# Performance work log

Hardware: AMD Instinct MI355X
Metric: run time of the kernel (lower is better)

Reference implementation:

```python
import jax, jax.numpy as jnp
import numpy as np

B, Q, KV = 4, 256, 1024
QS, KS, H, VS = 128, 128, 128, 256

def setup_inputs() -> dict:
    key = jax.random.key(0)
    ks = jax.random.split(key, 7)
    return {
        "queries": jax.random.normal(ks[0], (B, Q, QS), dtype=jnp.float32),
        "keys": jax.random.normal(ks[1], (B, KV, KS), dtype=jnp.float32),
        "values": jax.random.normal(ks[2], (B, KV, VS), dtype=jnp.float32),
        "valid_lens": jax.random.randint(ks[3], (B,), 0, KV, dtype=jnp.int64 if jax.config.read('jax_enable_x64') else jnp.int32),
        "Wq": jax.random.normal(ks[4], (QS, H), dtype=jnp.float32),
        "Wk": jax.random.normal(ks[5], (KS, H), dtype=jnp.float32),
        "wv": jax.random.normal(ks[6], (H,), dtype=jnp.float32),
    }

def reference(queries, keys, values, valid_lens, Wq, Wk, wv):
    # project: [B,Q,H], [B,KV,H]
    q = jnp.einsum('bqd,dh->bqh', queries, Wq)
    k = jnp.einsum('bkd,dh->bkh', keys, Wk)
    # additive scores: broadcast add -> tanh -> reduce with w_v  [B,Q,KV]
    feats = jnp.tanh(q[:, :, None, :] + k[:, None, :, :])  # [B,Q,KV,H]
    scores = jnp.einsum('bqkh,h->bqk', feats, wv)
    # masked softmax over KV with value -1e6 at masked slots
    mask = jnp.arange(scores.shape[-1])[None, None, :] < valid_lens[:, None, None]
    scores = jnp.where(mask, scores, -1e6)
    attn = jax.nn.softmax(scores, axis=-1)
    # weighted sum of values  [B,Q,VS]
    return jnp.einsum('bqk,bkv->bqv', attn, values)
```

## Files before the change

### kernel.cpp

```cpp
#include <hip/hip_runtime.h>

#define C2LOG2E 2.8853900817779268f
#define LOG2E   1.4426950408889634f

__device__ __forceinline__ float sig2(float x) {
    return __builtin_amdgcn_rcpf(__builtin_amdgcn_exp2f(x) + 1.0f);
}

__global__ __launch_bounds__(256) void proj_kernel(
    const float* __restrict__ q_in, const float* __restrict__ k_in,
    const float* __restrict__ Wq, const float* __restrict__ Wk,
    float* __restrict__ qc, float* __restrict__ kct)
{
    __shared__ __align__(16) float x_s[8][128];
    __shared__ float ps[2][8][128];
    int tid = threadIdx.x;
    int blk = blockIdx.x;
    bool is_q = (blk < 128);
    int r0 = (is_q ? blk : blk - 128) * 8;
    const float* X = (is_q ? q_in : k_in) + (size_t)r0 * 128;
    const float* W = is_q ? Wq : Wk;

    {
        float4 v = ((const float4*)X)[tid];
        *(float4*)&x_s[tid >> 5][(tid & 31) * 4] = v;
    }
    __syncthreads();

    int h    = tid & 127;
    int half = tid >> 7;
    int d0   = half * 64;
    float acc[8] = {0,0,0,0,0,0,0,0};
#pragma unroll 2
    for (int i4 = 0; i4 < 16; ++i4) {
        int d = d0 + 4*i4;
        float w0 = W[(d+0)*128 + h];
        float w1 = W[(d+1)*128 + h];
        float w2 = W[(d+2)*128 + h];
        float w3 = W[(d+3)*128 + h];
#pragma unroll
        for (int r = 0; r < 8; ++r) {
            float4 xv = *(const float4*)&x_s[r][d];
            acc[r] = fmaf(xv.x, w0, fmaf(xv.y, w1,
                     fmaf(xv.z, w2, fmaf(xv.w, w3, acc[r]))));
        }
    }
#pragma unroll
    for (int r = 0; r < 8; ++r) ps[half][r][h] = acc[r];
    __syncthreads();

    int rq = tid >> 7;
    float v0 = (ps[0][rq*4+0][h] + ps[1][rq*4+0][h]) * C2LOG2E;
    float v1 = (ps[0][rq*4+1][h] + ps[1][rq*4+1][h]) * C2LOG2E;
    float v2 = (ps[0][rq*4+2][h] + ps[1][rq*4+2][h]) * C2LOG2E;
    float v3 = (ps[0][rq*4+3][h] + ps[1][rq*4+3][h]) * C2LOG2E;

    if (is_q) {
        qc[(size_t)(r0 + rq*4 + 0)*128 + h] = v0;
        qc[(size_t)(r0 + rq*4 + 1)*128 + h] = v1;
        qc[(size_t)(r0 + rq*4 + 2)*128 + h] = v2;
        qc[(size_t)(r0 + rq*4 + 3)*128 + h] = v3;
    } else {
        int bb = r0 >> 10;
        int c  = (r0 & 1023) >> 6;
        int i0 = (r0 & 63) + rq*4;
        float* dst = kct + ((((size_t)(bb*16 + c))*32 + (h >> 2))*64 + i0)*4 + (h & 3);
        dst[0]  = v0;
        dst[4]  = v1;
        dst[8]  = v2;
        dst[12] = v3;
    }
}

__global__ __launch_bounds__(1024, 4) void attn_kernel(
    const float* __restrict__ qc, const float* __restrict__ kct,
    const float* __restrict__ values, const int* __restrict__ valid_lens,
    const float* __restrict__ wv, float* __restrict__ out)
{
    __shared__ float2 e2_s[2][1024];
    __shared__ float4 po8[8][4][64];
    __shared__ float2 red_m[16], red_s[16];

    int tid  = threadIdx.x;
    int b    = blockIdx.y;
    int q0   = blockIdx.x * 4;
    int w    = tid >> 6;
    int lane = tid & 63;
    int qh   = w >> 3;
    int c0   = w & 7;
    int vl   = valid_lens[b];

    const float4* qa4 = (const float4*)(qc + (size_t)(b*256 + q0 + 2*qh)*128);
    const float4* qb4 = qa4 + 32;
    const float4* wv4 = (const float4*)wv;
    const float4* kb  = (const float4*)kct;
    const float4* p0  = kb + ((size_t)(b*16 + c0))*2048 + lane;
    const float4* p1  = p0 + 8*2048;

    bool act0 = (c0*64 < vl);
    bool act1 = ((c0 + 8)*64 < vl);
    float a00=0.f, a10=0.f, a01=0.f, a11=0.f;

    if (act1) {
        for (int hb = 0; hb < 32; ++hb) {
            float4 wvv = wv4[hb];
            float4 qa = qa4[hb], qb = qb4[hb];
            float4 k0 = p0[(size_t)hb*64];
            float4 k1 = p1[(size_t)hb*64];
            a00 = fmaf(wvv.x, sig2(qa.x + k0.x), a00);
            a10 = fmaf(wvv.x, sig2(qb.x + k0.x), a10);
            a01 = fmaf(wvv.x, sig2(qa.x + k1.x), a01);
            a11 = fmaf(wvv.x, sig2(qb.x + k1.x), a11);
            a00 = fmaf(wvv.y, sig2(qa.y + k0.y), a00);
            a10 = fmaf(wvv.y, sig2(qb.y + k0.y), a10);
            a01 = fmaf(wvv.y, sig2(qa.y + k1.y), a01);
            a11 = fmaf(wvv.y, sig2(qb.y + k1.y), a11);
            a00 = fmaf(wvv.z, sig2(qa.z + k0.z), a00);
            a10 = fmaf(wvv.z, sig2(qb.z + k0.z), a10);
            a01 = fmaf(wvv.z, sig2(qa.z + k1.z), a01);
            a11 = fmaf(wvv.z, sig2(qb.z + k1.z), a11);
            a00 = fmaf(wvv.w, sig2(qa.w + k0.w), a00);
            a10 = fmaf(wvv.w, sig2(qb.w + k0.w), a10);
            a01 = fmaf(wvv.w, sig2(qa.w + k1.w), a01);
            a11 = fmaf(wvv.w, sig2(qb.w + k1.w), a11);
        }
    } else if (act0) {
        for (int hb = 0; hb < 32; ++hb) {
            float4 wvv = wv4[hb];
            float4 qa = qa4[hb], qb = qb4[hb];
            float4 k0 = p0[(size_t)hb*64];
            a00 = fmaf(wvv.x, sig2(qa.x + k0.x), a00);
            a10 = fmaf(wvv.x, sig2(qb.x + k0.x), a10);
            a00 = fmaf(wvv.y, sig2(qa.y + k0.y), a00);
            a10 = fmaf(wvv.y, sig2(qb.y + k0.y), a10);
            a00 = fmaf(wvv.z, sig2(qa.z + k0.z), a00);
            a10 = fmaf(wvv.z, sig2(qb.z + k0.z), a10);
            a00 = fmaf(wvv.w, sig2(qa.w + k0.w), a00);
            a10 = fmaf(wvv.w, sig2(qb.w + k0.w), a10);
        }
    }

    int kv0 = c0*64 + lane, kv1 = kv0 + 512;
    bool m0v = (kv0 < vl), m1v = (kv1 < vl);
    float s00 = m0v ? -2.f*a00 : -1e6f;
    float s10 = m0v ? -2.f*a10 : -1e6f;
    float s01 = m1v ? -2.f*a01 : -1e6f;
    float s11 = m1v ? -2.f*a11 : -1e6f;

    float m0 = fmaxf(s00, s01), m1 = fmaxf(s10, s11);
#pragma unroll
    for (int off = 32; off; off >>= 1) {
        m0 = fmaxf(m0, __shfl_xor(m0, off));
        m1 = fmaxf(m1, __shfl_xor(m1, off));
    }
    if (lane == 0) red_m[w] = make_float2(m0, m1);
    __syncthreads();
    {
        float2 mm = red_m[qh*8];
#pragma unroll
        for (int ww = 1; ww < 8; ++ww) {
            float2 t = red_m[qh*8 + ww];
            mm.x = fmaxf(mm.x, t.x); mm.y = fmaxf(mm.y, t.y);
        }
        m0 = mm.x; m1 = mm.y;
    }

    float e00 = __builtin_amdgcn_exp2f((s00 - m0) * LOG2E);
    float e10 = __builtin_amdgcn_exp2f((s10 - m1) * LOG2E);
    float e01 = __builtin_amdgcn_exp2f((s01 - m0) * LOG2E);
    float e11 = __builtin_amdgcn_exp2f((s11 - m1) * LOG2E);
    e2_s[qh][kv0] = make_float2(e00, e10);
    e2_s[qh][kv1] = make_float2(e01, e11);
    float l0 = e00 + e01, l1 = e10 + e11;
#pragma unroll
    for (int off = 32; off; off >>= 1) {
        l0 += __shfl_xor(l0, off);
        l1 += __shfl_xor(l1, off);
    }
    if (lane == 0) red_s[w] = make_float2(l0, l1);
    __syncthreads();

    int kv_end = (vl == 0) ? 1024 : vl;
    float4 ac[4] = {{0,0,0,0},{0,0,0,0},{0,0,0,0},{0,0,0,0}};
    const float4* V4 = (const float4*)values + (size_t)b*65536 + lane;
#pragma unroll 2
    for (int k2 = w; k2 < kv_end; k2 += 16) {
        float4 vv = V4[(size_t)k2*64];
        float2 ea = e2_s[0][k2];
        float2 eb = e2_s[1][k2];
        ac[0].x = fmaf(ea.x, vv.x, ac[0].x); ac[0].y = fmaf(ea.x, vv.y, ac[0].y);
        ac[0].z = fmaf(ea.x, vv.z, ac[0].z); ac[0].w = fmaf(ea.x, vv.w, ac[0].w);
        ac[1].x = fmaf(ea.y, vv.x, ac[1].x); ac[1].y = fmaf(ea.y, vv.y, ac[1].y);
        ac[1].z = fmaf(ea.y, vv.z, ac[1].z); ac[1].w = fmaf(ea.y, vv.w, ac[1].w);
        ac[2].x = fmaf(eb.x, vv.x, ac[2].x); ac[2].y = fmaf(eb.x, vv.y, ac[2].y);
        ac[2].z = fmaf(eb.x, vv.z, ac[2].z); ac[2].w = fmaf(eb.x, vv.w, ac[2].w);
        ac[3].x = fmaf(eb.y, vv.x, ac[3].x); ac[3].y = fmaf(eb.y, vv.y, ac[3].y);
        ac[3].z = fmaf(eb.y, vv.z, ac[3].z); ac[3].w = fmaf(eb.y, vv.w, ac[3].w);
    }

    if (w >= 8) {
#pragma unroll
        for (int q = 0; q < 4; ++q) po8[w-8][q][lane] = ac[q];
    }
    __syncthreads();
    if (w < 8) {
#pragma unroll
        for (int q = 0; q < 4; ++q) {
            float4 t = po8[w][q][lane];
            t.x += ac[q].x; t.y += ac[q].y; t.z += ac[q].z; t.w += ac[q].w;
            po8[w][q][lane] = t;
        }
    }
    __syncthreads();

    int qq  = tid >> 8;
    int col = tid & 255;
    float ssum = 0.f;
#pragma unroll
    for (int ww = 0; ww < 8; ++ww) {
        float2 t = red_s[(qq >> 1)*8 + ww];
        ssum += (qq & 1) ? t.y : t.x;
    }
    const float* pp = (const float*)po8;
    float r = 0.f;
#pragma unroll
    for (int ww = 0; ww < 8; ++ww) r += pp[(ww*4 + qq)*256 + col];
    out[((size_t)(b*256 + q0 + qq))*256 + col] = r / ssum;
}

extern "C" void kernel_launch(void* const* d_in, const int* in_sizes, int n_in,
                              void* d_out, int out_size, void* d_ws, size_t ws_size,
                              hipStream_t stream)
{
    const float* queries = (const float*)d_in[0];
    const float* keys    = (const float*)d_in[1];
    const float* values  = (const float*)d_in[2];
    const int*   vlens   = (const int*)d_in[3];
    const float* Wq      = (const float*)d_in[4];
    const float* Wk      = (const float*)d_in[5];
    const float* wv      = (const float*)d_in[6];
    float* out = (float*)d_out;

    float* qc  = (float*)d_ws;
    float* kct = qc + 4*256*128;

    proj_kernel<<<640, 256, 0, stream>>>(queries, keys, Wq, Wk, qc, kct);
    attn_kernel<<<dim3(64, 4), 1024, 0, stream>>>(qc, kct, values, vlens, wv, out);
}
```

Before: 103.2 us.

## Skip masked key projections, vectorize proj stores, halve attention block size

The projection kernel now returns early for key row-blocks beyond valid_len, skipping work whose scores are masked anyway. It also uses a 4-way split over input dimension with two output columns per thread, so results can be written as float4 stores in both the q and the transposed k layouts. The attention kernel goes from 1024-thread blocks covering 4 queries to 512-thread blocks covering 2 queries on a doubled grid, which drops the two-stage partial-sum reduction. The cost is that each V row is reread by twice as many blocks, and parallelism is restructured across the grid.

```diff
diff --git a/kernel.cpp b/kernel.cpp
--- a/kernel.cpp
+++ b/kernel.cpp
@@ -10,95 +10,95 @@
 __global__ __launch_bounds__(256) void proj_kernel(
     const float* __restrict__ q_in, const float* __restrict__ k_in,
     const float* __restrict__ Wq, const float* __restrict__ Wk,
+    const int* __restrict__ valid_lens,
     float* __restrict__ qc, float* __restrict__ kct)
 {
     __shared__ __align__(16) float x_s[8][128];
-    __shared__ float ps[2][8][128];
+    __shared__ __align__(16) float ps[4][8][128];
     int tid = threadIdx.x;
     int blk = blockIdx.x;
     bool is_q = (blk < 128);
     int r0 = (is_q ? blk : blk - 128) * 8;
+    int bb = r0 >> 10;
+    if (!is_q) {
+        int vl = valid_lens[bb];
+        if ((r0 & 1023) >= vl) return;
+    }
     const float* X = (is_q ? q_in : k_in) + (size_t)r0 * 128;
     const float* W = is_q ? Wq : Wk;
 
-    {
-        float4 v = ((const float4*)X)[tid];
-        *(float4*)&x_s[tid >> 5][(tid & 31) * 4] = v;
-    }
-    __syncthreads();
-
-    int h    = tid & 127;
-    int half = tid >> 7;
-    int d0   = half * 64;
-    float acc[8] = {0,0,0,0,0,0,0,0};
-#pragma unroll 2
-    for (int i4 = 0; i4 < 16; ++i4) {
-        int d = d0 + 4*i4;
-        float w0 = W[(d+0)*128 + h];
-        float w1 = W[(d+1)*128 + h];
-        float w2 = W[(d+2)*128 + h];
-        float w3 = W[(d+3)*128 + h];
+    *(float4*)&x_s[tid >> 5][(tid & 31) * 4] = ((const float4*)X)[tid];
+    __syncthreads();
+
+    int hl = tid & 63;
+    int dq = tid >> 6;
+    float a0[8] = {0,0,0,0,0,0,0,0};
+    float a1[8] = {0,0,0,0,0,0,0,0};
+#pragma unroll
+    for (int i4 = 0; i4 < 8; ++i4) {
+        int d = dq*32 + i4*4;
+        float w00 = W[(d+0)*128 + hl], w01 = W[(d+0)*128 + hl + 64];
+        float w10 = W[(d+1)*128 + hl], w11 = W[(d+1)*128 + hl + 64];
+        float w20 = W[(d+2)*128 + hl], w21 = W[(d+2)*128 + hl + 64];
+        float w30 = W[(d+3)*128 + hl], w31 = W[(d+3)*128 + hl + 64];
 #pragma unroll
         for (int r = 0; r < 8; ++r) {
             float4 xv = *(const float4*)&x_s[r][d];
-            acc[r] = fmaf(xv.x, w0, fmaf(xv.y, w1,
-                     fmaf(xv.z, w2, fmaf(xv.w, w3, acc[r]))));
-        }
-    }
-#pragma unroll
-    for (int r = 0; r < 8; ++r) ps[half][r][h] = acc[r];
-    __syncthreads();
-
-    int rq = tid >> 7;
-    float v0 = (ps[0][rq*4+0][h] + ps[1][rq*4+0][h]) * C2LOG2E;
-    float v1 = (ps[0][rq*4+1][h] + ps[1][rq*4+1][h]) * C2LOG2E;
-    float v2 = (ps[0][rq*4+2][h] + ps[1][rq*4+2][h]) * C2LOG2E;
-    float v3 = (ps[0][rq*4+3][h] + ps[1][rq*4+3][h]) * C2LOG2E;
-
+            a0[r] = fmaf(xv.x,w00, fmaf(xv.y,w10, fmaf(xv.z,w20, fmaf(xv.w,w30, a0[r]))));
+            a1[r] = fmaf(xv.x,w01, fmaf(xv.y,w11, fmaf(xv.z,w21, fmaf(xv.w,w31, a1[r]))));
+        }
+    }
+#pragma unroll
+    for (int r = 0; r < 8; ++r) {
+        ps[dq][r][hl]      = a0[r];
+        ps[dq][r][hl + 64] = a1[r];
+    }
+    __syncthreads();
+
+    int r  = tid >> 5;
+    int c4 = (tid & 31) * 4;
+    float4 s0 = *(const float4*)&ps[0][r][c4];
+    float4 s1 = *(const float4*)&ps[1][r][c4];
+    float4 s2 = *(const float4*)&ps[2][r][c4];
+    float4 s3 = *(const float4*)&ps[3][r][c4];
+    float4 v = make_float4(((s0.x+s1.x)+(s2.x+s3.x))*C2LOG2E,
+                           ((s0.y+s1.y)+(s2.y+s3.y))*C2LOG2E,
+                           ((s0.z+s1.z)+(s2.z+s3.z))*C2LOG2E,
+                           ((s0.w+s1.w)+(s2.w+s3.w))*C2LOG2E);
     if (is_q) {
-        qc[(size_t)(r0 + rq*4 + 0)*128 + h] = v0;
-        qc[(size_t)(r0 + rq*4 + 1)*128 + h] = v1;
-        qc[(size_t)(r0 + rq*4 + 2)*128 + h] = v2;
-        qc[(size_t)(r0 + rq*4 + 3)*128 + h] = v3;
+        *(float4*)&qc[(size_t)(r0 + r)*128 + c4] = v;
     } else {
-        int bb = r0 >> 10;
-        int c  = (r0 & 1023) >> 6;
-        int i0 = (r0 & 63) + rq*4;
-        float* dst = kct + ((((size_t)(bb*16 + c))*32 + (h >> 2))*64 + i0)*4 + (h & 3);
-        dst[0]  = v0;
-        dst[4]  = v1;
-        dst[8]  = v2;
-        dst[12] = v3;
-    }
-}
-
-__global__ __launch_bounds__(1024, 4) void attn_kernel(
+        int c    = (r0 & 1023) >> 6;
+        int kvin = (r0 & 63) + r;
+        *(float4*)&kct[((((size_t)(bb*16 + c))*32 + (c4 >> 2))*64 + kvin)*4] = v;
+    }
+}
+
+__global__ __launch_bounds__(512, 4) void attn_kernel(
     const float* __restrict__ qc, const float* __restrict__ kct,
     const float* __restrict__ values, const int* __restrict__ valid_lens,
     const float* __restrict__ wv, float* __restrict__ out)
 {
-    __shared__ float2 e2_s[2][1024];
-    __shared__ float4 po8[8][4][64];
-    __shared__ float2 red_m[16], red_s[16];
+    __shared__ float2 e2_s[1024];
+    __shared__ float4 po[8][2][64];
+    __shared__ float2 red_m[8], red_s[8];
 
     int tid  = threadIdx.x;
     int b    = blockIdx.y;
-    int q0   = blockIdx.x * 4;
+    int q0   = blockIdx.x * 2;
     int w    = tid >> 6;
     int lane = tid & 63;
-    int qh   = w >> 3;
-    int c0   = w & 7;
     int vl   = valid_lens[b];
 
-    const float4* qa4 = (const float4*)(qc + (size_t)(b*256 + q0 + 2*qh)*128);
+    const float4* qa4 = (const float4*)(qc + (size_t)(b*256 + q0)*128);
     const float4* qb4 = qa4 + 32;
     const float4* wv4 = (const float4*)wv;
     const float4* kb  = (const float4*)kct;
-    const float4* p0  = kb + ((size_t)(b*16 + c0))*2048 + lane;
+    const float4* p0  = kb + ((size_t)(b*16 + w))*2048 + lane;
     const float4* p1  = p0 + 8*2048;
 
-    bool act0 = (c0*64 < vl);
-    bool act1 = ((c0 + 8)*64 < vl);
+    bool act0 = (w*64 < vl);
+    bool act1 = ((w + 8)*64 < vl);
     float a00=0.f, a10=0.f, a01=0.f, a11=0.f;
 
     if (act1) {
@@ -140,7 +140,7 @@
         }
     }
 
-    int kv0 = c0*64 + lane, kv1 = kv0 + 512;
+    int kv0 = w*64 + lane, kv1 = kv0 + 512;
     bool m0v = (kv0 < vl), m1v = (kv1 < vl);
     float s00 = m0v ? -2.f*a00 : -1e6f;
     float s10 = m0v ? -2.f*a10 : -1e6f;
@@ -156,10 +156,10 @@
     if (lane == 0) red_m[w] = make_float2(m0, m1);
     __syncthreads();
     {
-        float2 mm = red_m[qh*8];
+        float2 mm = red_m[0];
 #pragma unroll
         for (int ww = 1; ww < 8; ++ww) {
-            float2 t = red_m[qh*8 + ww];
+            float2 t = red_m[ww];
             mm.x = fmaxf(mm.x, t.x); mm.y = fmaxf(mm.y, t.y);
         }
         m0 = mm.x; m1 = mm.y;
@@ -169,8 +169,8 @@
     float e10 = __builtin_amdgcn_exp2f((s10 - m1) * LOG2E);
     float e01 = __builtin_amdgcn_exp2f((s01 - m0) * LOG2E);
     float e11 = __builtin_amdgcn_exp2f((s11 - m1) * LOG2E);
-    e2_s[qh][kv0] = make_float2(e00, e10);
-    e2_s[qh][kv1] = make_float2(e01, e11);
+    e2_s[kv0] = make_float2(e00, e10);
+    e2_s[kv1] = make_float2(e01, e11);
     float l0 = e00 + e01, l1 = e10 + e11;
 #pragma unroll
     for (int off = 32; off; off >>= 1) {
@@ -181,36 +181,19 @@
     __syncthreads();
 
     int kv_end = (vl == 0) ? 1024 : vl;
-    float4 ac[4] = {{0,0,0,0},{0,0,0,0},{0,0,0,0},{0,0,0,0}};
+    float4 ac0 = {0,0,0,0}, ac1 = {0,0,0,0};
     const float4* V4 = (const float4*)values + (size_t)b*65536 + lane;
 #pragma unroll 2
-    for (int k2 = w; k2 < kv_end; k2 += 16) {
+    for (int k2 = w; k2 < kv_end; k2 += 8) {
         float4 vv = V4[(size_t)k2*64];
-        float2 ea = e2_s[0][k2];
-        float2 eb = e2_s[1][k2];
-        ac[0].x = fmaf(ea.x, vv.x, ac[0].x); ac[0].y = fmaf(ea.x, vv.y, ac[0].y);
-        ac[0].z = fmaf(ea.x, vv.z, ac[0].z); ac[0].w = fmaf(ea.x, vv.w, ac[0].w);
-        ac[1].x = fmaf(ea.y, vv.x, ac[1].x); ac[1].y = fmaf(ea.y, vv.y, ac[1].y);
-        ac[1].z = fmaf(ea.y, vv.z, ac[1].z); ac[1].w = fmaf(ea.y, vv.w, ac[1].w);
-        ac[2].x = fmaf(eb.x, vv.x, ac[2].x); ac[2].y = fmaf(eb.x, vv.y, ac[2].y);
-        ac[2].z = fmaf(eb.x, vv.z, ac[2].z); ac[2].w = fmaf(eb.x, vv.w, ac[2].w);
-        ac[3].x = fmaf(eb.y, vv.x, ac[3].x); ac[3].y = fmaf(eb.y, vv.y, ac[3].y);
-        ac[3].z = fmaf(eb.y, vv.z, ac[3].z); ac[3].w = fmaf(eb.y, vv.w, ac[3].w);
-    }
-
-    if (w >= 8) {
-#pragma unroll
-        for (int q = 0; q < 4; ++q) po8[w-8][q][lane] = ac[q];
-    }
-    __syncthreads();
-    if (w < 8) {
-#pragma unroll
-        for (int q = 0; q < 4; ++q) {
-            float4 t = po8[w][q][lane];
-            t.x += ac[q].x; t.y += ac[q].y; t.z += ac[q].z; t.w += ac[q].w;
-            po8[w][q][lane] = t;
-        }
-    }
+        float2 ee = e2_s[k2];
+        ac0.x = fmaf(ee.x, vv.x, ac0.x); ac0.y = fmaf(ee.x, vv.y, ac0.y);
+        ac0.z = fmaf(ee.x, vv.z, ac0.z); ac0.w = fmaf(ee.x, vv.w, ac0.w);
+        ac1.x = fmaf(ee.y, vv.x, ac1.x); ac1.y = fmaf(ee.y, vv.y, ac1.y);
+        ac1.z = fmaf(ee.y, vv.z, ac1.z); ac1.w = fmaf(ee.y, vv.w, ac1.w);
+    }
+    po[w][0][lane] = ac0;
+    po[w][1][lane] = ac1;
     __syncthreads();
 
     int qq  = tid >> 8;
@@ -218,13 +201,13 @@
     float ssum = 0.f;
 #pragma unroll
     for (int ww = 0; ww < 8; ++ww) {
-        float2 t = red_s[(qq >> 1)*8 + ww];
-        ssum += (qq & 1) ? t.y : t.x;
-    }
-    const float* pp = (const float*)po8;
+        float2 t = red_s[ww];
+        ssum += qq ? t.y : t.x;
+    }
+    const float* pp = (const float*)po;
     float r = 0.f;
 #pragma unroll
-    for (int ww = 0; ww < 8; ++ww) r += pp[(ww*4 + qq)*256 + col];
+    for (int ww = 0; ww < 8; ++ww) r += pp[(ww*2 + qq)*256 + col];
     out[((size_t)(b*256 + q0 + qq))*256 + col] = r / ssum;
 }
 
@@ -244,6 +227,6 @@
     float* qc  = (float*)d_ws;
     float* kct = qc + 4*256*128;
 
-    proj_kernel<<<640, 256, 0, stream>>>(queries, keys, Wq, Wk, qc, kct);
-    attn_kernel<<<dim3(64, 4), 1024, 0, stream>>>(qc, kct, values, vlens, wv, out);
-}
+    proj_kernel<<<640, 256, 0, stream>>>(queries, keys, Wq, Wk, vlens, qc, kct);
+    attn_kernel<<<dim3(128, 4), 512, 0, stream>>>(qc, kct, values, vlens, wv, out);
+}
```

New measurement: 99.62 us. -3.5%, faster.
